# Optimization experiments

Hardware: AMD Instinct MI355X
Metric: run time of the kernel (lower is better)

The kernel has to match this reference:

```python
import jax, jax.numpy as jnp
import numpy as np

N = 50000          # nodes
E = 800000         # directed edges (before self-loops)
HID = 64           # hidden_dim
HEADS = 4          # conv1 heads
NUM_CLASSES = 16
SLOPE = 0.2        # PyG GATConv default negative_slope


def setup_inputs() -> dict:
    key = jax.random.key(0)
    ks = jax.random.split(key, 10)
    s1 = 1.0 / np.sqrt(HID)
    s2 = 1.0 / np.sqrt(HEADS * HID)
    return {
        "x": jax.random.normal(ks[0], (N, HID), jnp.float32),
        "edge_index": jax.random.randint(ks[1], (2, E), 0, N, dtype=jnp.int64),
        # conv1: GATConv(64 -> 64, heads=4, concat)
        "W1": jax.random.normal(ks[2], (HID, HEADS * HID), jnp.float32) * s1,
        "att_src1": jax.random.normal(ks[3], (HEADS, HID), jnp.float32) * s1,
        "att_dst1": jax.random.normal(ks[4], (HEADS, HID), jnp.float32) * s1,
        "b1": jnp.zeros((HEADS * HID,), jnp.float32),
        # conv2: GATConv(256 -> num_classes, heads=1, concat)
        "W2": jax.random.normal(ks[5], (HEADS * HID, NUM_CLASSES), jnp.float32) * s2,
        "att_src2": jax.random.normal(ks[6], (1, NUM_CLASSES), jnp.float32) * s2,
        "att_dst2": jax.random.normal(ks[7], (1, NUM_CLASSES), jnp.float32) * s2,
        "b2": jnp.zeros((NUM_CLASSES,), jnp.float32),
    }


def _gat_conv(x, src, dst, W, att_s, att_d, b, heads, out_dim):
    # x: [N, F_in]; src/dst: [E'] with self-loops (PyG add_self_loops=True)
    xh = (x @ W).reshape(-1, heads, out_dim)                 # [N, H, D]
    a_src = jnp.einsum('nhd,hd->nh', xh, att_s)              # [N, H]
    a_dst = jnp.einsum('nhd,hd->nh', xh, att_d)              # [N, H]
    e = a_src[src] + a_dst[dst]                              # [E', H]
    e = jnp.where(e > 0, e, SLOPE * e)                       # leaky_relu(0.2)
    # segment softmax over incoming edges of each dst node
    m = jax.lax.stop_gradient(jax.ops.segment_max(e, dst, num_segments=N))
    ex = jnp.exp(e - m[dst])
    denom = jax.ops.segment_sum(ex, dst, num_segments=N)
    alpha = ex / (denom[dst] + 1e-16)                        # [E', H]
    out = jax.ops.segment_sum(xh[src] * alpha[:, :, None], dst, num_segments=N)
    return out.reshape(N, heads * out_dim) + b


def reference(x, edge_index, W1, att_src1, att_dst1, b1, W2, att_src2, att_dst2, b2):
    loops = jnp.arange(N, dtype=edge_index.dtype)
    src = jnp.concatenate([edge_index[0], loops])
    dst = jnp.concatenate([edge_index[1], loops])
    h = _gat_conv(x, src, dst, W1, att_src1, att_dst1, b1, HEADS, HID)
    h = jax.nn.elu(h)
    # F.dropout(p=0.5, training=False) -> identity at inference
    h = _gat_conv(h, src, dst, W2, att_src2, att_dst2, b2, 1, NUM_CLASSES)
    return jax.nn.log_softmax(h, axis=1)
```

## Files before the change

### kernel.cpp

```cpp
#include <hip/hip_runtime.h>
#include <hip/hip_bf16.h>
#include <math.h>

#define N_NODES 50000
#define N_EDGES 800000
#define EP (N_EDGES + N_NODES)
#define HID 64
#define HEADS 4
#define F1 (HEADS * HID)
#define NC 16
#define SLOPE 0.2f
#define NRT 3125
#define GMB 512
#define NT 49

typedef __attribute__((ext_vector_type(8))) short short8;
typedef __attribute__((ext_vector_type(4))) float f32x4;

__device__ __forceinline__ unsigned short bf16rn(float f) {
    unsigned u = __float_as_uint(f);
    return (unsigned short)((u + 0x7fffu + ((u >> 16) & 1u)) >> 16);
}
__device__ __forceinline__ float bf_lo(unsigned p) { return __uint_as_float(p << 16); }
__device__ __forceinline__ float bf_hi(unsigned p) { return __uint_as_float(p & 0xffff0000u); }

__device__ __forceinline__ void edge_sd(int e, const int* __restrict__ ei, int& s, int& d) {
    if (e < N_EDGES) { s = ei[e]; d = ei[N_EDGES + e]; }
    else             { s = e - N_EDGES; d = s; }
}

__global__ __launch_bounds__(1024) void k_scan_local(const int* __restrict__ cnt,
        int* __restrict__ lexcl, int* __restrict__ bsum) {
    __shared__ int wsum[16];
    int t = threadIdx.x, lane = t & 63, wid = t >> 6;
    int i = blockIdx.x * 1024 + t;
    int v = (i < N_NODES) ? cnt[i] : 0;
    int s = v;
#pragma unroll
    for (int off = 1; off < 64; off <<= 1) {
        int x = __shfl_up(s, off);
        if (lane >= off) s += x;
    }
    if (lane == 63) wsum[wid] = s;
    __syncthreads();
    if (t < 16) {
        int w = wsum[t];
#pragma unroll
        for (int off = 1; off < 16; off <<= 1) {
            int x = __shfl_up(w, off);
            if (t >= off) w += x;
        }
        wsum[t] = w;
    }
    __syncthreads();
    int waveoff = (wid == 0) ? 0 : wsum[wid - 1];
    int incl = s + waveoff;
    if (i < N_NODES) lexcl[i] = incl - v;
    if (t == 1023) bsum[blockIdx.x] = incl;
}

__global__ __launch_bounds__(256) void k_scan_add(int* __restrict__ row_start,
        const int* __restrict__ bsum, int* __restrict__ cursor) {
    __shared__ int sb[64];
    __shared__ int stot;
    int t = threadIdx.x;
    if (t < 64) {
        int v = (t < NT) ? bsum[t] : 0;
        int s = v;
#pragma unroll
        for (int off = 1; off < 64; off <<= 1) {
            int x = __shfl_up(s, off);
            if (t >= off) s += x;
        }
        sb[t] = s - v;
        if (t == 63) stot = s;
    }
    __syncthreads();
    int i = blockIdx.x * 256 + t;
    if (i < N_NODES) {
        int v = row_start[i] + sb[i >> 10];
        row_start[i] = v;
        cursor[i] = v;
    }
    if (i == 0) row_start[N_NODES] = stot;
}

__global__ void k_scatter(const int* __restrict__ ei, int* __restrict__ cursor,
                          int* __restrict__ esrc) {
    int e = blockIdx.x * blockDim.x + threadIdx.x;
    if (e >= EP) return;
    int s, d; edge_sd(e, ei, s, d);
    int p = atomicAdd(&cursor[d], 1);
    esrc[p] = s;
}

__global__ __launch_bounds__(256) void k_gemm1(
        const float* __restrict__ x, const float* __restrict__ W1,
        const float* __restrict__ att_s, const float* __restrict__ att_d,
        unsigned short* __restrict__ xh1b, float* __restrict__ a_src, float* __restrict__ a_dst,
        const int* __restrict__ ei, int* __restrict__ cnt) {
    __shared__ float xs[16][68];
    int t = threadIdx.x;
    for (int e = blockIdx.x * 256 + t; e < EP; e += 256 * GMB) {
        int s, d; edge_sd(e, ei, s, d);
        atomicAdd(&cnt[d], 1);
    }
    int w = t >> 6, l = t & 63;
    int lo16 = l & 15, kg = l >> 4;
    short8 bfrag[4][2];
#pragma unroll
    for (int ct = 0; ct < 4; ++ct)
#pragma unroll
        for (int kh = 0; kh < 2; ++kh) {
            const float* wp = W1 + (size_t)(kh * 32 + kg * 8) * F1 + (w * 64 + ct * 16 + lo16);
            short8 f;
#pragma unroll
            for (int i = 0; i < 8; ++i) f[i] = (short)bf16rn(wp[(size_t)i * F1]);
            bfrag[ct][kh] = f;
        }
    float asv[4], adv[4];
#pragma unroll
    for (int ct = 0; ct < 4; ++ct) {
        asv[ct] = att_s[w * 64 + ct * 16 + lo16];
        adv[ct] = att_d[w * 64 + ct * 16 + lo16];
    }
    int sr = t >> 4, sc = (t & 15) * 4;
    for (int rt = blockIdx.x; rt < NRT; rt += GMB) {
        __syncthreads();
        *(float4*)&xs[sr][sc] = *(const float4*)(x + (size_t)(rt * 16 + sr) * HID + sc);
        __syncthreads();
        short8 af[2];
#pragma unroll
        for (int kh = 0; kh < 2; ++kh) {
            const float* xp = &xs[lo16][kh * 32 + kg * 8];
            float4 u0 = *(const float4*)xp;
            float4 u1 = *(const float4*)(xp + 4);
            short8 f;
            f[0] = (short)bf16rn(u0.x); f[1] = (short)bf16rn(u0.y);
            f[2] = (short)bf16rn(u0.z); f[3] = (short)bf16rn(u0.w);
            f[4] = (short)bf16rn(u1.x); f[5] = (short)bf16rn(u1.y);
            f[6] = (short)bf16rn(u1.z); f[7] = (short)bf16rn(u1.w);
            af[kh] = f;
        }
        f32x4 acc[4];
#pragma unroll
        for (int ct = 0; ct < 4; ++ct) {
            acc[ct] = (f32x4){0.f, 0.f, 0.f, 0.f};
            acc[ct] = __builtin_amdgcn_mfma_f32_16x16x32_bf16(af[0], bfrag[ct][0], acc[ct], 0, 0, 0);
            acc[ct] = __builtin_amdgcn_mfma_f32_16x16x32_bf16(af[1], bfrag[ct][1], acc[ct], 0, 0, 0);
        }
#pragma unroll
        for (int reg = 0; reg < 4; ++reg) {
            int gr = rt * 16 + kg * 4 + reg;
#pragma unroll
            for (int ct = 0; ct < 4; ++ct)
                xh1b[(size_t)gr * F1 + w * 64 + ct * 16 + lo16] = bf16rn(acc[ct][reg]);
            float ps = acc[0][reg] * asv[0] + acc[1][reg] * asv[1]
                     + acc[2][reg] * asv[2] + acc[3][reg] * asv[3];
            float pd = acc[0][reg] * adv[0] + acc[1][reg] * adv[1]
                     + acc[2][reg] * adv[2] + acc[3][reg] * adv[3];
#pragma unroll
            for (int o = 1; o <= 8; o <<= 1) {
                ps += __shfl_xor(ps, o);
                pd += __shfl_xor(pd, o);
            }
            if (lo16 == 0) {
                a_src[gr * HEADS + w] = ps;
                a_dst[gr * HEADS + w] = pd;
            }
        }
    }
}

__global__ __launch_bounds__(256) void k_csr1(
        const int* __restrict__ row_start, const int* __restrict__ esrc,
        const float* __restrict__ a_src, const float* __restrict__ a_dst,
        const unsigned short* __restrict__ xh1b, const float* __restrict__ b1,
        const float* __restrict__ W2, const float* __restrict__ att_s2,
        const float* __restrict__ att_d2,
        unsigned short* __restrict__ xh2b, float* __restrict__ a_src2,
        float* __restrict__ a_dst2) {
    int w = threadIdx.x >> 6, l = threadIdx.x & 63;
    int d = blockIdx.x * 4 + w;
    if (d >= N_NODES) return;
    int base = row_start[d], deg = row_start[d + 1] - base;
    __shared__ int   ls[4][64];
    __shared__ float lal[4][4][64];
    int h = l >> 4, e16 = l & 15;
    int* lsw = ls[w];
    float adh = a_dst[d * HEADS + h];
    float m = -1e30f, den = 0.0f;
    float a0 = 0.0f, a1 = 0.0f, a2 = 0.0f, a3 = 0.0f;
    for (int c0 = 0; c0 < deg; c0 += 64) {
        int cn = min(64, deg - c0);
        if (l < cn) lsw[l] = esrc[base + c0 + l];
        float cm = -1e30f;
        for (int j = e16; j < cn; j += 16) {
            float ev = a_src[lsw[j] * HEADS + h] + adh;
            ev = ev > 0.0f ? ev : SLOPE * ev;
            lal[w][h][j] = ev;
            cm = fmaxf(cm, ev);
        }
#pragma unroll
        for (int o = 8; o >= 1; o >>= 1) cm = fmaxf(cm, __shfl_xor(cm, o));
        float mn = fmaxf(m, cm);
        float sc = expf(m - mn);
        a0 *= sc; a1 *= sc; a2 *= sc; a3 *= sc; den *= sc; m = mn;
        float cs = 0.0f;
        for (int j = e16; j < cn; j += 16) {
            float wj = expf(lal[w][h][j] - m);
            lal[w][h][j] = wj;
            cs += wj;
        }
#pragma unroll
        for (int o = 8; o >= 1; o >>= 1) cs += __shfl_xor(cs, o);
        den += cs;
        const float* lalh = lal[w][h];
        int j = 0;
        for (; j + 1 < cn; j += 2) {
            float w0 = lalh[j], w1 = lalh[j + 1];
            uint2 p0 = *(const uint2*)(xh1b + (size_t)lsw[j]     * F1 + 4 * l);
            uint2 p1 = *(const uint2*)(xh1b + (size_t)lsw[j + 1] * F1 + 4 * l);
            a0 += w0 * bf_lo(p0.x); a1 += w0 * bf_hi(p0.x);
            a2 += w0 * bf_lo(p0.y); a3 += w0 * bf_hi(p0.y);
            a0 += w1 * bf_lo(p1.x); a1 += w1 * bf_hi(p1.x);
            a2 += w1 * bf_lo(p1.y); a3 += w1 * bf_hi(p1.y);
        }
        if (j < cn) {
            float w0 = lalh[j];
            uint2 p0 = *(const uint2*)(xh1b + (size_t)lsw[j] * F1 + 4 * l);
            a0 += w0 * bf_lo(p0.x); a1 += w0 * bf_hi(p0.x);
            a2 += w0 * bf_lo(p0.y); a3 += w0 * bf_hi(p0.y);
        }
    }
    float inv = 1.0f / (den + 1e-16f);
    float4 bb = *(const float4*)(b1 + 4 * l);
    float v0 = a0 * inv + bb.x;
    float v1 = a1 * inv + bb.y;
    float v2 = a2 * inv + bb.z;
    float v3 = a3 * inv + bb.w;
    v0 = v0 > 0.0f ? v0 : (expf(v0) - 1.0f);
    v1 = v1 > 0.0f ? v1 : (expf(v1) - 1.0f);
    v2 = v2 > 0.0f ? v2 : (expf(v2) - 1.0f);
    v3 = v3 > 0.0f ? v3 : (expf(v3) - 1.0f);
    float* hrow = &lal[w][0][0];
    *(float4*)(hrow + 4 * l) = make_float4(v0, v1, v2, v3);
    int k0 = l >> 2;
    int cg = (l & 3) * 4;
    const float4* w4 = (const float4*)W2;
    float q0 = 0.0f, q1 = 0.0f, q2 = 0.0f, q3 = 0.0f;
#pragma unroll
    for (int j = 0; j < 16; ++j) {
        float hk = hrow[k0 + 16 * j];
        float4 wv = w4[l + 64 * j];
        q0 += hk * wv.x; q1 += hk * wv.y; q2 += hk * wv.z; q3 += hk * wv.w;
    }
#pragma unroll
    for (int o = 4; o <= 32; o <<= 1) {
        q0 += __shfl_xor(q0, o); q1 += __shfl_xor(q1, o);
        q2 += __shfl_xor(q2, o); q3 += __shfl_xor(q3, o);
    }
    if (l < 4) {
        unsigned u0 = (unsigned)bf16rn(q0) | ((unsigned)bf16rn(q1) << 16);
        unsigned u1 = (unsigned)bf16rn(q2) | ((unsigned)bf16rn(q3) << 16);
        *(uint2*)(xh2b + (size_t)d * NC + 4 * l) = make_uint2(u0, u1);
        float ps = q0 * att_s2[cg] + q1 * att_s2[cg + 1]
                 + q2 * att_s2[cg + 2] + q3 * att_s2[cg + 3];
        float pd = q0 * att_d2[cg] + q1 * att_d2[cg + 1]
                 + q2 * att_d2[cg + 2] + q3 * att_d2[cg + 3];
        ps += __shfl_xor(ps, 1); ps += __shfl_xor(ps, 2);
        pd += __shfl_xor(pd, 1); pd += __shfl_xor(pd, 2);
        if (l == 0) { a_src2[d] = ps; a_dst2[d] = pd; }
    }
}

__global__ __launch_bounds__(256) void k_csr2(
        const int* __restrict__ row_start, const int* __restrict__ esrc,
        const float* __restrict__ a_src2, const float* __restrict__ a_dst2,
        const unsigned short* __restrict__ xh2b, const float* __restrict__ b2,
        float* __restrict__ out) {
    int w = threadIdx.x >> 6, l = threadIdx.x & 63;
    int d = blockIdx.x * 4 + w;
    if (d >= N_NODES) return;
    int base = row_start[d], deg = row_start[d + 1] - base;
    __shared__ int   ls[4][64];
    __shared__ float lal[4][64];
    float adh = a_dst2[d];
    int cp = l & 7, je = l >> 3;
    float denl = 0.0f, acc0 = 0.0f, acc1 = 0.0f;
    for (int c0 = 0; c0 < deg; c0 += 64) {
        int cn = min(64, deg - c0);
        if (l < cn) {
            int s = esrc[base + c0 + l];
            ls[w][l] = s;
            float ev = a_src2[s] + adh;
            ev = ev > 0.0f ? ev : SLOPE * ev;
            float wj = __expf(ev);
            lal[w][l] = wj;
            denl += wj;
        }
        for (int j = je; j < cn; j += 8) {
            float wj = lal[w][j];
            unsigned pv = *(const unsigned*)(xh2b + (size_t)ls[w][j] * NC + 2 * cp);
            acc0 += wj * bf_lo(pv);
            acc1 += wj * bf_hi(pv);
        }
    }
#pragma unroll
    for (int o = 32; o >= 1; o >>= 1) denl += __shfl_xor(denl, o);
#pragma unroll
    for (int o = 8; o <= 32; o <<= 1) {
        acc0 += __shfl_xor(acc0, o);
        acc1 += __shfl_xor(acc1, o);
    }
    float inv = 1.0f / (denl + 1e-16f);
    float v0 = acc0 * inv + b2[2 * cp];
    float v1 = acc1 * inv + b2[2 * cp + 1];
    float mm = fmaxf(v0, v1);
#pragma unroll
    for (int o = 1; o <= 4; o <<= 1) mm = fmaxf(mm, __shfl_xor(mm, o));
    float se = __expf(v0 - mm) + __expf(v1 - mm);
#pragma unroll
    for (int o = 1; o <= 4; o <<= 1) se += __shfl_xor(se, o);
    float lse = mm + logf(se);
    if (l < 8) *(float2*)(out + (size_t)d * NC + 2 * cp) = make_float2(v0 - lse, v1 - lse);
}

extern "C" void kernel_launch(void* const* d_in, const int* in_sizes, int n_in,
                              void* d_out, int out_size, void* d_ws, size_t ws_size,
                              hipStream_t stream) {
    const float* x        = (const float*)d_in[0];
    const int*   ei       = (const int*)d_in[1];
    const float* W1       = (const float*)d_in[2];
    const float* att_src1 = (const float*)d_in[3];
    const float* att_dst1 = (const float*)d_in[4];
    const float* b1       = (const float*)d_in[5];
    const float* W2       = (const float*)d_in[6];
    const float* att_src2 = (const float*)d_in[7];
    const float* att_dst2 = (const float*)d_in[8];
    const float* b2       = (const float*)d_in[9];
    float* out = (float*)d_out;

    char* p = (char*)d_ws;
    unsigned short* xh1b  = (unsigned short*)p; p += (size_t)N_NODES * F1 * 2;
    unsigned short* xh2b  = (unsigned short*)p; p += (size_t)N_NODES * NC * 2;
    float* a_src1 = (float*)p; p += (size_t)N_NODES * HEADS * 4;
    float* a_dst1 = (float*)p; p += (size_t)N_NODES * HEADS * 4;
    float* a_src2 = (float*)p; p += (size_t)N_NODES * 4;
    float* a_dst2 = (float*)p; p += (size_t)N_NODES * 4;
    int* cnt       = (int*)p;  p += (size_t)N_NODES * 4;
    int* cursor    = (int*)p;  p += (size_t)N_NODES * 4;
    int* row_start = (int*)p;  p += (size_t)(N_NODES + 1) * 4;
    int* bsum      = (int*)p;  p += 64 * 4;
    int* esrc      = (int*)p;  p += (size_t)EP * 4;

    hipMemsetAsync(cnt, 0, (size_t)N_NODES * 4, stream);
    k_gemm1<<<GMB, 256, 0, stream>>>(x, W1, att_src1, att_dst1, xh1b, a_src1, a_dst1,
                                     ei, cnt);
    k_scan_local<<<NT, 1024, 0, stream>>>(cnt, row_start, bsum);
    k_scan_add<<<(N_NODES + 255) / 256, 256, 0, stream>>>(row_start, bsum, cursor);
    k_scatter<<<(EP + 255) / 256, 256, 0, stream>>>(ei, cursor, esrc);

    k_csr1<<<(N_NODES + 3) / 4, 256, 0, stream>>>(row_start, esrc, a_src1, a_dst1, xh1b, b1,
                                                  W2, att_src2, att_dst2, xh2b, a_src2, a_dst2);

    k_csr2<<<(N_NODES + 3) / 4, 256, 0, stream>>>(row_start, esrc, a_src2, a_dst2, xh2b, b2, out);
}
```

Before: 214.7 us.

## Widen GAT edge gathers to 16-byte loads and drop online-softmax max pass

In the first-layer aggregation, each lane now gathers 8 bf16 features with 16-byte loads. The two half-waves process alternate edges and are combined by a cross-half shuffle at the end. The online max/rescale softmax is replaced by a single pass that uses __expf without max subtraction, which removes a pass over the edge chunk and the rescaling work. In the second layer, each lane now loads 4 classes with 8-byte loads and fewer lanes per edge. Dropping the max subtraction risks overflow if attention logits grow large.

```diff
diff --git a/kernel.cpp b/kernel.cpp
--- a/kernel.cpp
+++ b/kernel.cpp
@@ -187,64 +187,80 @@
     __shared__ int   ls[4][64];
     __shared__ float lal[4][4][64];
     int h = l >> 4, e16 = l & 15;
+    int eoff = l >> 5, fl = l & 31, hf = fl >> 3;
     int* lsw = ls[w];
     float adh = a_dst[d * HEADS + h];
-    float m = -1e30f, den = 0.0f;
-    float a0 = 0.0f, a1 = 0.0f, a2 = 0.0f, a3 = 0.0f;
+    float denl = 0.0f;
+    float a0=0.f,a1=0.f,a2=0.f,a3=0.f,a4=0.f,a5=0.f,a6=0.f,a7=0.f;
     for (int c0 = 0; c0 < deg; c0 += 64) {
         int cn = min(64, deg - c0);
         if (l < cn) lsw[l] = esrc[base + c0 + l];
-        float cm = -1e30f;
         for (int j = e16; j < cn; j += 16) {
             float ev = a_src[lsw[j] * HEADS + h] + adh;
             ev = ev > 0.0f ? ev : SLOPE * ev;
-            lal[w][h][j] = ev;
-            cm = fmaxf(cm, ev);
-        }
-#pragma unroll
-        for (int o = 8; o >= 1; o >>= 1) cm = fmaxf(cm, __shfl_xor(cm, o));
-        float mn = fmaxf(m, cm);
-        float sc = expf(m - mn);
-        a0 *= sc; a1 *= sc; a2 *= sc; a3 *= sc; den *= sc; m = mn;
-        float cs = 0.0f;
-        for (int j = e16; j < cn; j += 16) {
-            float wj = expf(lal[w][h][j] - m);
+            float wj = __expf(ev);
             lal[w][h][j] = wj;
-            cs += wj;
-        }
-#pragma unroll
-        for (int o = 8; o >= 1; o >>= 1) cs += __shfl_xor(cs, o);
-        den += cs;
-        const float* lalh = lal[w][h];
+            denl += wj;
+        }
+        const float* lalh = lal[w][hf];
         int j = 0;
+        for (; j + 3 < cn; j += 4) {
+            float wa = lalh[j + eoff], wb = lalh[j + 2 + eoff];
+            uint4 pa = *(const uint4*)(xh1b + (size_t)lsw[j + eoff]     * F1 + 8 * fl);
+            uint4 pb = *(const uint4*)(xh1b + (size_t)lsw[j + 2 + eoff] * F1 + 8 * fl);
+            a0 += wa * bf_lo(pa.x); a1 += wa * bf_hi(pa.x);
+            a2 += wa * bf_lo(pa.y); a3 += wa * bf_hi(pa.y);
+            a4 += wa * bf_lo(pa.z); a5 += wa * bf_hi(pa.z);
+            a6 += wa * bf_lo(pa.w); a7 += wa * bf_hi(pa.w);
+            a0 += wb * bf_lo(pb.x); a1 += wb * bf_hi(pb.x);
+            a2 += wb * bf_lo(pb.y); a3 += wb * bf_hi(pb.y);
+            a4 += wb * bf_lo(pb.z); a5 += wb * bf_hi(pb.z);
+            a6 += wb * bf_lo(pb.w); a7 += wb * bf_hi(pb.w);
+        }
         for (; j + 1 < cn; j += 2) {
-            float w0 = lalh[j], w1 = lalh[j + 1];
-            uint2 p0 = *(const uint2*)(xh1b + (size_t)lsw[j]     * F1 + 4 * l);
-            uint2 p1 = *(const uint2*)(xh1b + (size_t)lsw[j + 1] * F1 + 4 * l);
-            a0 += w0 * bf_lo(p0.x); a1 += w0 * bf_hi(p0.x);
-            a2 += w0 * bf_lo(p0.y); a3 += w0 * bf_hi(p0.y);
-            a0 += w1 * bf_lo(p1.x); a1 += w1 * bf_hi(p1.x);
-            a2 += w1 * bf_lo(p1.y); a3 += w1 * bf_hi(p1.y);
-        }
-        if (j < cn) {
-            float w0 = lalh[j];
-            uint2 p0 = *(const uint2*)(xh1b + (size_t)lsw[j] * F1 + 4 * l);
-            a0 += w0 * bf_lo(p0.x); a1 += w0 * bf_hi(p0.x);
-            a2 += w0 * bf_lo(p0.y); a3 += w0 * bf_hi(p0.y);
-        }
-    }
-    float inv = 1.0f / (den + 1e-16f);
-    float4 bb = *(const float4*)(b1 + 4 * l);
-    float v0 = a0 * inv + bb.x;
-    float v1 = a1 * inv + bb.y;
-    float v2 = a2 * inv + bb.z;
-    float v3 = a3 * inv + bb.w;
-    v0 = v0 > 0.0f ? v0 : (expf(v0) - 1.0f);
-    v1 = v1 > 0.0f ? v1 : (expf(v1) - 1.0f);
-    v2 = v2 > 0.0f ? v2 : (expf(v2) - 1.0f);
-    v3 = v3 > 0.0f ? v3 : (expf(v3) - 1.0f);
+            float wa = lalh[j + eoff];
+            uint4 pa = *(const uint4*)(xh1b + (size_t)lsw[j + eoff] * F1 + 8 * fl);
+            a0 += wa * bf_lo(pa.x); a1 += wa * bf_hi(pa.x);
+            a2 += wa * bf_lo(pa.y); a3 += wa * bf_hi(pa.y);
+            a4 += wa * bf_lo(pa.z); a5 += wa * bf_hi(pa.z);
+            a6 += wa * bf_lo(pa.w); a7 += wa * bf_hi(pa.w);
+        }
+        if (j < cn && eoff == 0) {
+            float wa = lalh[j];
+            uint4 pa = *(const uint4*)(xh1b + (size_t)lsw[j] * F1 + 8 * fl);
+            a0 += wa * bf_lo(pa.x); a1 += wa * bf_hi(pa.x);
+            a2 += wa * bf_lo(pa.y); a3 += wa * bf_hi(pa.y);
+            a4 += wa * bf_lo(pa.z); a5 += wa * bf_hi(pa.z);
+            a6 += wa * bf_lo(pa.w); a7 += wa * bf_hi(pa.w);
+        }
+    }
+#pragma unroll
+    for (int o = 8; o >= 1; o >>= 1) denl += __shfl_xor(denl, o);
+    float dd = __shfl(denl, hf * 16);
+    float inv = 1.0f / (dd + 1e-16f);
+    a0 += __shfl_xor(a0, 32); a1 += __shfl_xor(a1, 32);
+    a2 += __shfl_xor(a2, 32); a3 += __shfl_xor(a3, 32);
+    a4 += __shfl_xor(a4, 32); a5 += __shfl_xor(a5, 32);
+    a6 += __shfl_xor(a6, 32); a7 += __shfl_xor(a7, 32);
+    float4 bb0 = *(const float4*)(b1 + 8 * fl);
+    float4 bb1 = *(const float4*)(b1 + 8 * fl + 4);
+    float v0 = a0 * inv + bb0.x, v1 = a1 * inv + bb0.y;
+    float v2 = a2 * inv + bb0.z, v3 = a3 * inv + bb0.w;
+    float v4 = a4 * inv + bb1.x, v5 = a5 * inv + bb1.y;
+    float v6 = a6 * inv + bb1.z, v7 = a7 * inv + bb1.w;
+    v0 = v0 > 0.0f ? v0 : (__expf(v0) - 1.0f);
+    v1 = v1 > 0.0f ? v1 : (__expf(v1) - 1.0f);
+    v2 = v2 > 0.0f ? v2 : (__expf(v2) - 1.0f);
+    v3 = v3 > 0.0f ? v3 : (__expf(v3) - 1.0f);
+    v4 = v4 > 0.0f ? v4 : (__expf(v4) - 1.0f);
+    v5 = v5 > 0.0f ? v5 : (__expf(v5) - 1.0f);
+    v6 = v6 > 0.0f ? v6 : (__expf(v6) - 1.0f);
+    v7 = v7 > 0.0f ? v7 : (__expf(v7) - 1.0f);
     float* hrow = &lal[w][0][0];
-    *(float4*)(hrow + 4 * l) = make_float4(v0, v1, v2, v3);
+    if (l < 32) {
+        *(float4*)(hrow + 8 * fl)     = make_float4(v0, v1, v2, v3);
+        *(float4*)(hrow + 8 * fl + 4) = make_float4(v4, v5, v6, v7);
+    }
     int k0 = l >> 2;
     int cg = (l & 3) * 4;
     const float4* w4 = (const float4*)W2;
@@ -286,8 +302,8 @@
     __shared__ int   ls[4][64];
     __shared__ float lal[4][64];
     float adh = a_dst2[d];
-    int cp = l & 7, je = l >> 3;
-    float denl = 0.0f, acc0 = 0.0f, acc1 = 0.0f;
+    int cp4 = l & 3, je = l >> 2;
+    float denl = 0.0f, a0 = 0.0f, a1 = 0.0f, a2 = 0.0f, a3 = 0.0f;
     for (int c0 = 0; c0 < deg; c0 += 64) {
         int cn = min(64, deg - c0);
         if (l < cn) {
@@ -299,31 +315,34 @@
             lal[w][l] = wj;
             denl += wj;
         }
-        for (int j = je; j < cn; j += 8) {
+        for (int j = je; j < cn; j += 16) {
             float wj = lal[w][j];
-            unsigned pv = *(const unsigned*)(xh2b + (size_t)ls[w][j] * NC + 2 * cp);
-            acc0 += wj * bf_lo(pv);
-            acc1 += wj * bf_hi(pv);
+            uint2 pv = *(const uint2*)(xh2b + (size_t)ls[w][j] * NC + 4 * cp4);
+            a0 += wj * bf_lo(pv.x); a1 += wj * bf_hi(pv.x);
+            a2 += wj * bf_lo(pv.y); a3 += wj * bf_hi(pv.y);
         }
     }
 #pragma unroll
     for (int o = 32; o >= 1; o >>= 1) denl += __shfl_xor(denl, o);
 #pragma unroll
-    for (int o = 8; o <= 32; o <<= 1) {
-        acc0 += __shfl_xor(acc0, o);
-        acc1 += __shfl_xor(acc1, o);
+    for (int o = 4; o <= 32; o <<= 1) {
+        a0 += __shfl_xor(a0, o); a1 += __shfl_xor(a1, o);
+        a2 += __shfl_xor(a2, o); a3 += __shfl_xor(a3, o);
     }
     float inv = 1.0f / (denl + 1e-16f);
-    float v0 = acc0 * inv + b2[2 * cp];
-    float v1 = acc1 * inv + b2[2 * cp + 1];
-    float mm = fmaxf(v0, v1);
-#pragma unroll
-    for (int o = 1; o <= 4; o <<= 1) mm = fmaxf(mm, __shfl_xor(mm, o));
-    float se = __expf(v0 - mm) + __expf(v1 - mm);
-#pragma unroll
-    for (int o = 1; o <= 4; o <<= 1) se += __shfl_xor(se, o);
+    float v0 = a0 * inv + b2[4 * cp4 + 0];
+    float v1 = a1 * inv + b2[4 * cp4 + 1];
+    float v2 = a2 * inv + b2[4 * cp4 + 2];
+    float v3 = a3 * inv + b2[4 * cp4 + 3];
+    float mm = fmaxf(fmaxf(v0, v1), fmaxf(v2, v3));
+    mm = fmaxf(mm, __shfl_xor(mm, 1));
+    mm = fmaxf(mm, __shfl_xor(mm, 2));
+    float se = __expf(v0 - mm) + __expf(v1 - mm) + __expf(v2 - mm) + __expf(v3 - mm);
+    se += __shfl_xor(se, 1);
+    se += __shfl_xor(se, 2);
     float lse = mm + logf(se);
-    if (l < 8) *(float2*)(out + (size_t)d * NC + 2 * cp) = make_float2(v0 - lse, v1 - lse);
+    if (l < 4) *(float4*)(out + (size_t)d * NC + 4 * l)
+                   = make_float4(v0 - lse, v1 - lse, v2 - lse, v3 - lse);
 }
 
 extern "C" void kernel_launch(void* const* d_in, const int* in_sizes, int n_in,
```

After: 207.2 us. 3.5% less time.
